# Kernel optimization log

Hardware: AMD Instinct MI355X
Metric: run time of the kernel (lower is better)

## Reference

```python
import jax, jax.numpy as jnp
import numpy as np

B_SZ, L, D_MODEL, D_STATE, D_CONV, EXPAND = 8, 2048, 512, 16, 4, 2
D_INNER = EXPAND * D_MODEL
DT_RANK = (D_MODEL + 15) // 16  # 32
ENC_IN, MARK_IN, C_OUT, PRED_LEN = 7, 4, 7, 96
IN_SIZE = ENC_IN + MARK_IN


def setup_inputs() -> dict:
    key = jax.random.key(0)
    ks = jax.random.split(key, 16)
    s = 0.02
    inp = {
        "x_enc": jax.random.normal(ks[0], (B_SZ, L, ENC_IN), jnp.float32),
        "x_mark_enc": jax.random.normal(ks[1], (B_SZ, L, MARK_IN), jnp.float32),
        "x_dec": jax.random.normal(ks[2], (B_SZ, PRED_LEN, ENC_IN), jnp.float32),
        "x_mark_dec": jax.random.normal(ks[3], (B_SZ, PRED_LEN, MARK_IN), jnp.float32),
        # input_transform
        "W_in": jax.random.normal(ks[4], (IN_SIZE, D_MODEL), jnp.float32) * s,
        "b_in": jnp.zeros((D_MODEL,), jnp.float32),
        # mamba in_proj (no bias)
        "W_inproj": jax.random.normal(ks[5], (D_MODEL, 2 * D_INNER), jnp.float32) * s,
        # depthwise causal conv
        "conv_w": jax.random.normal(ks[6], (D_INNER, D_CONV), jnp.float32) * s,
        "conv_b": jnp.zeros((D_INNER,), jnp.float32),
        # x_proj -> dt, B, C (no bias)
        "W_xproj": jax.random.normal(ks[7], (D_INNER, DT_RANK + 2 * D_STATE), jnp.float32) * s,
        # dt_proj
        "W_dt": jax.random.normal(ks[8], (DT_RANK, D_INNER), jnp.float32) * s,
        "b_dt": jnp.log(jnp.expm1(jnp.full((D_INNER,), 0.01, jnp.float32))),  # softplus-inv of ~0.01
        # S4D real init
        "A_log": jnp.log(jnp.broadcast_to(jnp.arange(1, D_STATE + 1, dtype=jnp.float32), (D_INNER, D_STATE))),
        "D": jnp.ones((D_INNER,), jnp.float32),
        # out_proj (no bias)
        "W_out": jax.random.normal(ks[9], (D_INNER, D_MODEL), jnp.float32) * s,
        # head
        "W_fc": jax.random.normal(ks[10], (D_MODEL, C_OUT), jnp.float32) * s,
        "b_fc": jnp.zeros((C_OUT,), jnp.float32),
    }
    return inp


def _mamba(x, W_inproj, conv_w, conv_b, W_xproj, W_dt, b_dt, A_log, D, W_out):
    # x: (B, L, d_model)
    xz = x @ W_inproj                      # (B, L, 2*d_inner)
    u, z = jnp.split(xz, 2, axis=-1)       # each (B, L, d_inner)
    # causal depthwise conv over time
    u_t = jnp.transpose(u, (0, 2, 1))      # (B, d_inner, L)
    conv = jax.lax.conv_general_dilated(
        u_t, conv_w[:, None, :], (1,), [(D_CONV - 1, 0)],
        dimension_numbers=("NCH", "OIH", "NCH"), feature_group_count=D_INNER)
    u = jax.nn.silu(jnp.transpose(conv, (0, 2, 1)) + conv_b)  # (B, L, d_inner)

    x_dbl = u @ W_xproj                    # (B, L, dt_rank + 2*d_state)
    dt_lo, Bmat, Cmat = jnp.split(x_dbl, [DT_RANK, DT_RANK + D_STATE], axis=-1)
    dt = jax.nn.softplus(dt_lo @ W_dt + b_dt)  # (B, L, d_inner)
    A = -jnp.exp(A_log)                    # (d_inner, d_state)

    def step(h, inp):
        dt_t, B_t, C_t, u_t = inp          # (B,d_inner),(B,d_state),(B,d_state),(B,d_inner)
        dA = jnp.exp(dt_t[:, :, None] * A)                       # (B, d_inner, d_state)
        dBu = dt_t[:, :, None] * B_t[:, None, :] * u_t[:, :, None]
        h = dA * h + dBu
        y = jnp.einsum("bds,bs->bd", h, C_t) + D * u_t
        return h, y

    h0 = jnp.zeros((x.shape[0], D_INNER, D_STATE), x.dtype)
    xs = (jnp.swapaxes(dt, 0, 1), jnp.swapaxes(Bmat, 0, 1),
          jnp.swapaxes(Cmat, 0, 1), jnp.swapaxes(u, 0, 1))
    _, ys = jax.lax.scan(step, h0, xs)     # ys: (L, B, d_inner)
    y = jnp.swapaxes(ys, 0, 1) * jax.nn.silu(z)
    return y @ W_out                       # (B, L, d_model)


def reference(x_enc, x_mark_enc, x_dec, x_mark_dec, W_in, b_in, W_inproj,
              conv_w, conv_b, W_xproj, W_dt, b_dt, A_log, D, W_out, W_fc, b_fc):
    x = jnp.concatenate([x_enc, x_mark_enc], axis=-1) @ W_in + b_in  # (B, L, d_model)
    x = _mamba(x, W_inproj, conv_w, conv_b, W_xproj, W_dt, b_dt, A_log, D, W_out)
    return x[:, -PRED_LEN:, :] @ W_fc + b_fc  # (B, pred_len, c_out)
```

## Files before the change

kernel.cpp:

```cpp
#include <hip/hip_runtime.h>
#include <math.h>

#define BB 8
#define LL 2048
#define DI 1024
#define NS 16
#define RK 32
#define NI 11
#define PRED 96
#define NC 7

static constexpr size_t OFF_WF   = 0;
static constexpr size_t OFF_BF   = 22528;
static constexpr size_t OFF_A2   = 24576;
static constexpr size_t OFF_WOF  = 40960;
static constexpr size_t OFF_CWT  = 48128;
static constexpr size_t OFF_WXH  = 52224;
static constexpr size_t OFF_WDTH = 84992;
static constexpr size_t OFF_DLH  = 101376;
static constexpr size_t OFF_BC   = 363520;
static constexpr size_t OFF_CC   = 625664;
static constexpr size_t OFF_YS   = 887808;
static constexpr size_t OFF_PB   = 1674240;
static constexpr size_t OFF_HB   = 5868544;
static constexpr size_t OFF_UH   = 10324992;

typedef __attribute__((ext_vector_type(8))) __bf16 bf16x8;
typedef __attribute__((ext_vector_type(8))) _Float16 f16x8;
typedef __attribute__((ext_vector_type(4))) float f32x4;

__device__ __forceinline__ float fexp2(float x) {
#if __has_builtin(__builtin_amdgcn_exp2f)
  return __builtin_amdgcn_exp2f(x);
#else
  return exp2f(x);
#endif
}
__device__ __forceinline__ unsigned short f2bf(float f) {
  unsigned int b = __float_as_uint(f);
  unsigned int r = (b + 0x7fffu + ((b >> 16) & 1u)) >> 16;
  return (unsigned short)r;
}
__device__ __forceinline__ unsigned short f2h_u(float f) {
  union { _Float16 h; unsigned short u; } c;
  c.h = (_Float16)f;
  return c.u;
}
__device__ __forceinline__ float h2f(unsigned short u) {
  union { unsigned short u; _Float16 h; } c;
  c.u = u;
  return (float)c.h;
}
__device__ __forceinline__ float softp(float a) {
  return (a > 15.f) ? a : __logf(1.f + __expf(a));
}

__global__ __launch_bounds__(256) void k_pre(
    const float* __restrict__ W_in, const float* __restrict__ b_in,
    const float* __restrict__ W_inproj, const float* __restrict__ conv_w,
    const float* __restrict__ W_xproj, const float* __restrict__ W_dt,
    const float* __restrict__ A_log,
    const float* __restrict__ W_out, const float* __restrict__ W_fc,
    float* __restrict__ ws) {
  int bid = blockIdx.x, tid = threadIdx.x;
  if (bid < 96) {
    int out = bid * 256 + tid;
    int r = out >> 11, c = out & 2047;
    const float* arow = (r < NI) ? (W_in + (size_t)r * 512) : b_in;
    float a0 = 0.f, a1 = 0.f, a2 = 0.f, a3 = 0.f;
    for (int k = 0; k < 512; k += 4) {
      a0 = fmaf(arow[k + 0], W_inproj[(size_t)(k + 0) * 2048 + c], a0);
      a1 = fmaf(arow[k + 1], W_inproj[(size_t)(k + 1) * 2048 + c], a1);
      a2 = fmaf(arow[k + 2], W_inproj[(size_t)(k + 2) * 2048 + c], a2);
      a3 = fmaf(arow[k + 3], W_inproj[(size_t)(k + 3) * 2048 + c], a3);
    }
    float acc = (a0 + a1) + (a2 + a3);
    if (r < NI) ws[OFF_WF + (size_t)r * 2048 + c] = acc;
    else ws[OFF_BF + c] = acc;
  } else if (bid < 160) {
    int idx = (bid - 96) * 256 + tid;
    ws[OFF_A2 + idx] = -expf(A_log[idx]) * 1.4426950408889634f;
  } else if (bid < 188) {
    int out = (bid - 160) * 256 + tid;
    int d = out / NC, cc = out - d * NC;
    float a0 = 0.f, a1 = 0.f, a2 = 0.f, a3 = 0.f;
    for (int k = 0; k < 512; k += 4) {
      a0 = fmaf(W_out[(size_t)d * 512 + k + 0], W_fc[(k + 0) * NC + cc], a0);
      a1 = fmaf(W_out[(size_t)d * 512 + k + 1], W_fc[(k + 1) * NC + cc], a1);
      a2 = fmaf(W_out[(size_t)d * 512 + k + 2], W_fc[(k + 2) * NC + cc], a2);
      a3 = fmaf(W_out[(size_t)d * 512 + k + 3], W_fc[(k + 3) * NC + cc], a3);
    }
    ws[OFF_WOF + out] = (a0 + a1) + (a2 + a3);
  } else if (bid < 204) {
    int idx = (bid - 188) * 256 + tid;
    int k = idx >> 10, dd = idx & 1023;
    ws[OFF_CWT + idx] = conv_w[dd * 4 + k];
  } else if (bid < 460) {
    int idx = (bid - 204) * 256 + tid;
    int c = idx >> 10, k = idx & 1023;
    unsigned short* wxh = (unsigned short*)(ws + OFF_WXH);
    wxh[idx] = f2bf(W_xproj[(size_t)k * 64 + c]);
  } else {
    int idx = (bid - 460) * 256 + tid;
    int dd = idx >> 5, k = idx & 31;
    unsigned short* wdh = (unsigned short*)(ws + OFF_WDTH);
    wdh[idx] = f2h_u(W_dt[(size_t)k * DI + dd]);
  }
}

__global__ __launch_bounds__(256) void k_u(
    const float* __restrict__ xe, const float* __restrict__ xm,
    const float* __restrict__ conv_b, float* __restrict__ ws) {
  __shared__ float scat[11][11];
  int bid = blockIdx.x, tid = threadIdx.x;
  int tg = bid >> 2, dq = bid & 3;
  int d = dq * 256 + tid;
  int b = tg >> 8;
  int t0 = (tg & 255) * 8;
  if (tid < 121) {
    int k = tid / 11, i = tid - k * 11;
    int tp = t0 - 3 + k;
    float v = 0.f;
    if (tp >= 0) v = (i < 7) ? xe[(size_t)(b * LL + tp) * 7 + i]
                             : xm[(size_t)(b * LL + tp) * 4 + (i - 7)];
    scat[k][i] = v;
  }
  __syncthreads();
  float wfv[NI];
#pragma unroll
  for (int i = 0; i < NI; ++i) wfv[i] = ws[OFF_WF + (size_t)i * 2048 + d];
  float bfu = ws[OFF_BF + d];
  float cwv[4];
#pragma unroll
  for (int k = 0; k < 4; ++k) cwv[k] = ws[OFF_CWT + k * 1024 + d];
  float cbv = conv_b[d];
  float xzv[11];
#pragma unroll
  for (int w2 = 0; w2 < 11; ++w2) {
    int tp = t0 - 3 + w2;
    float xz = bfu;
#pragma unroll
    for (int i = 0; i < NI; ++i) xz = fmaf(scat[w2][i], wfv[i], xz);
    xzv[w2] = (tp >= 0) ? xz : 0.f;
  }
  unsigned short* uhp = (unsigned short*)(ws + OFF_UH);
#pragma unroll
  for (int tt = 0; tt < 8; ++tt) {
    float acc = cbv;
#pragma unroll
    for (int k = 0; k < 4; ++k) acc = fmaf(cwv[k], xzv[tt + k], acc);
    float uval = acc / (1.f + __expf(-acc));
    uhp[(size_t)(b * LL + t0 + tt) * DI + d] = f2bf(uval);
  }
}

__global__ __launch_bounds__(256) void k_proj(float* __restrict__ ws) {
  __shared__ unsigned short su[64][72];
  __shared__ unsigned short sw[64][72];
  const unsigned short* uh  = (const unsigned short*)(ws + OFF_UH);
  const unsigned short* wxh = (const unsigned short*)(ws + OFF_WXH);
  int bid = blockIdx.x, tid = threadIdx.x;
  int r0 = bid * 64;
  int lane = tid & 63, w = tid >> 6;
  int srow = tid >> 3, skg = tid & 7;
  uint4 ru[2][2], rw[2][2];
  const ushort* ub0 = uh + (size_t)(r0 + srow) * DI + skg * 8;
  const ushort* wb0 = wxh + (size_t)srow * DI + skg * 8;
  ru[0][0] = *(const uint4*)(ub0);
  ru[0][1] = *(const uint4*)(ub0 + (size_t)32 * DI);
  rw[0][0] = *(const uint4*)(wb0);
  rw[0][1] = *(const uint4*)(wb0 + (size_t)32 * DI);
  ru[1][0] = *(const uint4*)(ub0 + 64);
  ru[1][1] = *(const uint4*)(ub0 + (size_t)32 * DI + 64);
  rw[1][0] = *(const uint4*)(wb0 + 64);
  rw[1][1] = *(const uint4*)(wb0 + (size_t)32 * DI + 64);
  f32x4 acc[4];
#pragma unroll
  for (int i = 0; i < 4; ++i) acc[i] = (f32x4){0.f, 0.f, 0.f, 0.f};
  int arow = w * 16 + (lane & 15);
  for (int kt = 0; kt < 16; ++kt) {
    int set = kt & 1;
    __syncthreads();
    *(uint4*)&su[srow][skg * 8]      = ru[set][0];
    *(uint4*)&su[srow + 32][skg * 8] = ru[set][1];
    *(uint4*)&sw[srow][skg * 8]      = rw[set][0];
    *(uint4*)&sw[srow + 32][skg * 8] = rw[set][1];
    __syncthreads();
    if (kt + 2 < 16) {
      int ko = (kt + 2) * 64;
      ru[set][0] = *(const uint4*)(ub0 + ko);
      ru[set][1] = *(const uint4*)(ub0 + (size_t)32 * DI + ko);
      rw[set][0] = *(const uint4*)(wb0 + ko);
      rw[set][1] = *(const uint4*)(wb0 + (size_t)32 * DI + ko);
    }
#pragma unroll
    for (int ks = 0; ks < 2; ++ks) {
      int koff = ks * 32 + (lane >> 4) * 8;
      bf16x8 av = *(const bf16x8*)&su[arow][koff];
#pragma unroll
      for (int nt = 0; nt < 4; ++nt) {
        bf16x8 bv = *(const bf16x8*)&sw[nt * 16 + (lane & 15)][koff];
        acc[nt] = __builtin_amdgcn_mfma_f32_16x16x32_bf16(av, bv, acc[nt], 0, 0, 0);
      }
    }
  }
  int orow = r0 + w * 16 + ((lane >> 4) << 2);
  int ocol = lane & 15;
  unsigned short* dlh = (unsigned short*)(ws + OFF_DLH);
#pragma unroll
  for (int reg = 0; reg < 4; ++reg) {
    size_t rr = orow + reg;
    dlh[rr * 32 + ocol]      = f2h_u(acc[0][reg]);
    dlh[rr * 32 + 16 + ocol] = f2h_u(acc[1][reg]);
    ws[OFF_BC + rr * NS + ocol] = acc[2][reg];
    ws[OFF_CC + rr * NS + ocol] = acc[3][reg];
  }
}

__global__ __launch_bounds__(128) void k_scan1(
    const float* __restrict__ b_dt, float* __restrict__ ws) {
  __shared__ unsigned short sdt[64][128];
  __shared__ unsigned short suu[64][128];
  __shared__ float sBB[64][16];
  int bid = blockIdx.x, tid = threadIdx.x;
  int b = bid >> 8, dgrp = (bid >> 5) & 7, ch = bid & 31;
  int d0 = dgrp * 128, t0 = ch * 64;
  size_t row0 = (size_t)b * LL + t0;
  const unsigned short* uh  = (const unsigned short*)(ws + OFF_UH) + row0 * DI + d0;
  const unsigned short* dlh = (const unsigned short*)(ws + OFF_DLH) + row0 * 32;
  const unsigned short* wdh = (const unsigned short*)(ws + OFF_WDTH);
  const float* Bp = ws + OFF_BC + row0 * NS;
  {
    int row = tid >> 1, q0 = (tid & 1) * 8;
    const uint4* src = (const uint4*)(uh + (size_t)row * DI) + q0;
    uint4* dst = (uint4*)&suu[row][0] + q0;
#pragma unroll
    for (int j = 0; j < 8; ++j) dst[j] = src[j];
  }
#pragma unroll
  for (int j = 0; j < 2; ++j) {
    int slot = tid * 2 + j, row = slot >> 2, q = slot & 3;
    *(float4*)&sBB[row][q * 4] = *(const float4*)&Bp[(size_t)row * NS + q * 4];
  }
  __syncthreads();
  {
    int lane = tid & 63, w = tid >> 6;
    int cl = lane & 15, kg = lane >> 4;
#pragma unroll
    for (int i = 0; i < 2; ++i) {
      int tq = 2 * w + i;
      f16x8 af = *(const f16x8*)&dlh[(size_t)(tq * 16 + cl) * 32 + kg * 8];
#pragma unroll
      for (int dq = 0; dq < 8; ++dq) {
        int dcol = d0 + dq * 16 + cl;
        f16x8 bf8 = *(const f16x8*)&wdh[(size_t)dcol * 32 + kg * 8];
        f32x4 acc = (f32x4){0.f, 0.f, 0.f, 0.f};
        acc = __builtin_amdgcn_mfma_f32_16x16x32_f16(af, bf8, acc, 0, 0, 0);
        float bdt = b_dt[dcol];
#pragma unroll
        for (int r = 0; r < 4; ++r)
          sdt[tq * 16 + kg * 4 + r][dq * 16 + cl] = f2h_u(softp(acc[r] + bdt));
      }
    }
  }
  __syncthreads();
  int d = d0 + tid;
  float a20 = ws[OFF_A2 + (size_t)d * NS];
  float h[16];
#pragma unroll
  for (int s = 0; s < 16; ++s) h[s] = 0.f;
  float S = 0.f;
  for (int t = 0; t < 64; ++t) {
    float dtv = h2f(sdt[t][tid]);
    float uv  = __uint_as_float((unsigned)suu[t][tid] << 16);
    float dtu = dtv * uv;
    S += dtv;
    float e1 = fexp2(dtv * a20);
    f32x4 b0 = *(const f32x4*)&sBB[t][0];
    f32x4 b1 = *(const f32x4*)&sBB[t][4];
    f32x4 b2 = *(const f32x4*)&sBB[t][8];
    f32x4 b3 = *(const f32x4*)&sBB[t][12];
    float dA = e1;
    h[0]  = fmaf(dA, h[0],  b0[0] * dtu); dA *= e1;
    h[1]  = fmaf(dA, h[1],  b0[1] * dtu); dA *= e1;
    h[2]  = fmaf(dA, h[2],  b0[2] * dtu); dA *= e1;
    h[3]  = fmaf(dA, h[3],  b0[3] * dtu); dA *= e1;
    h[4]  = fmaf(dA, h[4],  b1[0] * dtu); dA *= e1;
    h[5]  = fmaf(dA, h[5],  b1[1] * dtu); dA *= e1;
    h[6]  = fmaf(dA, h[6],  b1[2] * dtu); dA *= e1;
    h[7]  = fmaf(dA, h[7],  b1[3] * dtu); dA *= e1;
    h[8]  = fmaf(dA, h[8],  b2[0] * dtu); dA *= e1;
    h[9]  = fmaf(dA, h[9],  b2[1] * dtu); dA *= e1;
    h[10] = fmaf(dA, h[10], b2[2] * dtu); dA *= e1;
    h[11] = fmaf(dA, h[11], b2[3] * dtu); dA *= e1;
    h[12] = fmaf(dA, h[12], b3[0] * dtu); dA *= e1;
    h[13] = fmaf(dA, h[13], b3[1] * dtu); dA *= e1;
    h[14] = fmaf(dA, h[14], b3[2] * dtu); dA *= e1;
    h[15] = fmaf(dA, h[15], b3[3] * dtu);
  }
  float E1 = fexp2(S * a20);
  float P[16];
  float pp = E1;
#pragma unroll
  for (int s = 0; s < 16; ++s) { P[s] = pp; pp *= E1; }
  size_t base = (((size_t)b * 32 + ch) * 1024 + d) * 16;
#pragma unroll
  for (int q = 0; q < 4; ++q) {
    *(float4*)&ws[OFF_PB + base + q * 4] = *(float4*)&P[q * 4];
    *(float4*)&ws[OFF_HB + base + q * 4] = *(float4*)&h[q * 4];
  }
}

__global__ __launch_bounds__(128) void k_tail(
    const float* __restrict__ b_dt, const float* __restrict__ Dvec,
    float* __restrict__ ws) {
  __shared__ unsigned short sdt[64][128];
  __shared__ unsigned short suu[64][128];
  __shared__ float sBB[64][16];
  __shared__ float sCC[64][16];
  int bid = blockIdx.x, tid = threadIdx.x;
  int b = bid >> 4, dgrp = (bid >> 1) & 7, half = bid & 1;
  int d0 = dgrp * 128, t0 = (30 + half) * 64;
  size_t row0 = (size_t)b * LL + t0;
  const unsigned short* uh  = (const unsigned short*)(ws + OFF_UH) + row0 * DI + d0;
  const unsigned short* dlh = (const unsigned short*)(ws + OFF_DLH) + row0 * 32;
  const unsigned short* wdh = (const unsigned short*)(ws + OFF_WDTH);
  const float* Bp = ws + OFF_BC + row0 * NS;
  const float* Cp = ws + OFF_CC + row0 * NS;
  int d = d0 + tid;
  {
    int row = tid >> 1, q0 = (tid & 1) * 8;
    const uint4* src = (const uint4*)(uh + (size_t)row * DI) + q0;
    uint4* dst = (uint4*)&suu[row][0] + q0;
#pragma unroll
    for (int j = 0; j < 8; ++j) dst[j] = src[j];
  }
#pragma unroll
  for (int j = 0; j < 2; ++j) {
    int slot = tid * 2 + j, row = slot >> 2, q = slot & 3;
    *(float4*)&sBB[row][q * 4] = *(const float4*)&Bp[(size_t)row * NS + q * 4];
    *(float4*)&sCC[row][q * 4] = *(const float4*)&Cp[(size_t)row * NS + q * 4];
  }
  float h[16];
#pragma unroll
  for (int s = 0; s < 16; ++s) h[s] = 0.f;
  int nch = 30 + half;
  for (int c = 0; c < nch; ++c) {
    size_t cb = (((size_t)b * 32 + c) * 1024 + d) * 16;
#pragma unroll
    for (int q = 0; q < 4; ++q) {
      f32x4 Pv = *(const f32x4*)&ws[OFF_PB + cb + q * 4];
      f32x4 Hv = *(const f32x4*)&ws[OFF_HB + cb + q * 4];
#pragma unroll
      for (int j = 0; j < 4; ++j)
        h[q * 4 + j] = fmaf(Pv[j], h[q * 4 + j], Hv[j]);
    }
  }
  __syncthreads();
  {
    int lane = tid & 63, w = tid >> 6;
    int cl = lane & 15, kg = lane >> 4;
#pragma unroll
    for (int i = 0; i < 2; ++i) {
      int tq = 2 * w + i;
      f16x8 af = *(const f16x8*)&dlh[(size_t)(tq * 16 + cl) * 32 + kg * 8];
#pragma unroll
      for (int dq = 0; dq < 8; ++dq) {
        int dcol = d0 + dq * 16 + cl;
        f16x8 bf8 = *(const f16x8*)&wdh[(size_t)dcol * 32 + kg * 8];
        f32x4 acc = (f32x4){0.f, 0.f, 0.f, 0.f};
        acc = __builtin_amdgcn_mfma_f32_16x16x32_f16(af, bf8, acc, 0, 0, 0);
        float bdt = b_dt[dcol];
#pragma unroll
        for (int r = 0; r < 4; ++r)
          sdt[tq * 16 + kg * 4 + r][dq * 16 + cl] = f2h_u(softp(acc[r] + bdt));
      }
    }
  }
  __syncthreads();
  float a20 = ws[OFF_A2 + (size_t)d * NS];
  float Dv = Dvec[d];
  float* ysp = ws + OFF_YS;
  int tstart = half ? 0 : 32;
  for (int t = 0; t < 64; ++t) {
    float dtv = h2f(sdt[t][tid]);
    float uv  = __uint_as_float((unsigned)suu[t][tid] << 16);
    float dtu = dtv * uv;
    float e1 = fexp2(dtv * a20);
    f32x4 b0 = *(const f32x4*)&sBB[t][0];
    f32x4 b1 = *(const f32x4*)&sBB[t][4];
    f32x4 b2 = *(const f32x4*)&sBB[t][8];
    f32x4 b3 = *(const f32x4*)&sBB[t][12];
    float dA = e1;
    h[0]  = fmaf(dA, h[0],  b0[0] * dtu); dA *= e1;
    h[1]  = fmaf(dA, h[1],  b0[1] * dtu); dA *= e1;
    h[2]  = fmaf(dA, h[2],  b0[2] * dtu); dA *= e1;
    h[3]  = fmaf(dA, h[3],  b0[3] * dtu); dA *= e1;
    h[4]  = fmaf(dA, h[4],  b1[0] * dtu); dA *= e1;
    h[5]  = fmaf(dA, h[5],  b1[1] * dtu); dA *= e1;
    h[6]  = fmaf(dA, h[6],  b1[2] * dtu); dA *= e1;
    h[7]  = fmaf(dA, h[7],  b1[3] * dtu); dA *= e1;
    h[8]  = fmaf(dA, h[8],  b2[0] * dtu); dA *= e1;
    h[9]  = fmaf(dA, h[9],  b2[1] * dtu); dA *= e1;
    h[10] = fmaf(dA, h[10], b2[2] * dtu); dA *= e1;
    h[11] = fmaf(dA, h[11], b2[3] * dtu); dA *= e1;
    h[12] = fmaf(dA, h[12], b3[0] * dtu); dA *= e1;
    h[13] = fmaf(dA, h[13], b3[1] * dtu); dA *= e1;
    h[14] = fmaf(dA, h[14], b3[2] * dtu); dA *= e1;
    h[15] = fmaf(dA, h[15], b3[3] * dtu);
    if (t >= tstart) {
      f32x4 c0 = *(const f32x4*)&sCC[t][0];
      f32x4 c1 = *(const f32x4*)&sCC[t][4];
      f32x4 c2 = *(const f32x4*)&sCC[t][8];
      f32x4 c3 = *(const f32x4*)&sCC[t][12];
      float pv = h[0] * c0[0] + h[1] * c0[1] + h[2] * c0[2] + h[3] * c0[3]
               + h[4] * c1[0] + h[5] * c1[1] + h[6] * c1[2] + h[7] * c1[3]
               + h[8] * c2[0] + h[9] * c2[1] + h[10] * c2[2] + h[11] * c2[3]
               + h[12] * c3[0] + h[13] * c3[1] + h[14] * c3[2] + h[15] * c3[3];
      ysp[((size_t)(b * PRED + (t0 + t - (LL - PRED)))) * DI + d] = fmaf(Dv, uv, pv);
    }
  }
}

__global__ __launch_bounds__(256) void k_out(
    const float* __restrict__ xe, const float* __restrict__ xm,
    const float* __restrict__ b_fc, const float* __restrict__ ws,
    float* __restrict__ out) {
  __shared__ float scat[NI];
  __shared__ float sacc[4][NC];
  int bid = blockIdx.x, tid = threadIdx.x;
  int b = bid / PRED, p = bid - b * PRED;
  int t = LL - PRED + p;
  if (tid < NI) scat[tid] = (tid < 7) ? xe[(size_t)(b * LL + t) * 7 + tid]
                                      : xm[(size_t)(b * LL + t) * 4 + (tid - 7)];
  __syncthreads();
  const float* Wf  = ws + OFF_WF;
  const float* bf  = ws + OFF_BF;
  const float* Wof = ws + OFF_WOF;
  const float* ysp = ws + OFF_YS + ((size_t)bid) * DI;
  float acc[NC];
#pragma unroll
  for (int cc = 0; cc < NC; ++cc) acc[cc] = 0.f;
#pragma unroll
  for (int j = 0; j < 4; ++j) {
    int dd = tid + j * 256;
    float zv = bf[DI + dd];
#pragma unroll
    for (int i = 0; i < NI; ++i) zv = fmaf(scat[i], Wf[(size_t)i * 2048 + DI + dd], zv);
    float g = ysp[dd] * (zv / (1.f + __expf(-zv)));
#pragma unroll
    for (int cc = 0; cc < NC; ++cc) acc[cc] = fmaf(g, Wof[dd * NC + cc], acc[cc]);
  }
#pragma unroll
  for (int cc = 0; cc < NC; ++cc) {
    float v = acc[cc];
    for (int off = 32; off > 0; off >>= 1) v += __shfl_down(v, off);
    if ((tid & 63) == 0) sacc[tid >> 6][cc] = v;
  }
  __syncthreads();
  if (tid < NC)
    out[(size_t)bid * NC + tid] =
        sacc[0][tid] + sacc[1][tid] + sacc[2][tid] + sacc[3][tid] + b_fc[tid];
}

extern "C" void kernel_launch(void* const* d_in, const int* in_sizes, int n_in,
                              void* d_out, int out_size, void* d_ws, size_t ws_size,
                              hipStream_t stream) {
  const float* xe    = (const float*)d_in[0];
  const float* xm    = (const float*)d_in[1];
  const float* W_in  = (const float*)d_in[4];
  const float* b_in  = (const float*)d_in[5];
  const float* W_ip  = (const float*)d_in[6];
  const float* cw    = (const float*)d_in[7];
  const float* cb    = (const float*)d_in[8];
  const float* W_xp  = (const float*)d_in[9];
  const float* W_dt  = (const float*)d_in[10];
  const float* b_dt  = (const float*)d_in[11];
  const float* A_log = (const float*)d_in[12];
  const float* Dv    = (const float*)d_in[13];
  const float* W_out = (const float*)d_in[14];
  const float* W_fc  = (const float*)d_in[15];
  const float* b_fc  = (const float*)d_in[16];
  float* ws  = (float*)d_ws;
  float* out = (float*)d_out;

  k_pre  <<<588, 256, 0, stream>>>(W_in, b_in, W_ip, cw, W_xp, W_dt, A_log, W_out, W_fc, ws);
  k_u    <<<8192, 256, 0, stream>>>(xe, xm, cb, ws);
  k_proj <<<256, 256, 0, stream>>>(ws);
  k_scan1<<<2048, 128, 0, stream>>>(b_dt, ws);
  k_tail <<<128, 128, 0, stream>>>(b_dt, Dv, ws);
  k_out  <<<BB * PRED, 256, 0, stream>>>(xe, xm, b_fc, ws, out);
}
```

Baseline: 171.1 us.

## Move dt projection into k_proj and split scan states across threads

Computes the dt_proj MFMA plus softplus once in k_proj and writes a full fp16 dt tensor to global memory. k_scan1 and k_tail then load it instead of redoing the projection per block. k_scan1 now runs 256 threads, with each half handling 8 of the 16 states and using pow8 powers in place of the serial dA chain, which cuts the dependency chain length and doubles thread parallelism. The chunk P/H buffers are transposed to a state-major layout so reads are coalesced across d. The cost is an extra 32 MB fp16 dt write and read through global memory.

```diff
diff --git a/kernel.cpp b/kernel.cpp
--- a/kernel.cpp
+++ b/kernel.cpp
@@ -17,13 +17,13 @@
 static constexpr size_t OFF_CWT  = 48128;
 static constexpr size_t OFF_WXH  = 52224;
 static constexpr size_t OFF_WDTH = 84992;
-static constexpr size_t OFF_DLH  = 101376;
-static constexpr size_t OFF_BC   = 363520;
-static constexpr size_t OFF_CC   = 625664;
-static constexpr size_t OFF_YS   = 887808;
-static constexpr size_t OFF_PB   = 1674240;
-static constexpr size_t OFF_HB   = 5868544;
-static constexpr size_t OFF_UH   = 10324992;
+static constexpr size_t OFF_BC   = 101376;
+static constexpr size_t OFF_CC   = 363520;
+static constexpr size_t OFF_YS   = 625664;
+static constexpr size_t OFF_PB   = 1412096;
+static constexpr size_t OFF_HB   = 5606400;
+static constexpr size_t OFF_UH   = 9800704;
+static constexpr size_t OFF_DT   = 18189312;
 
 typedef __attribute__((ext_vector_type(8))) __bf16 bf16x8;
 typedef __attribute__((ext_vector_type(8))) _Float16 f16x8;
@@ -53,6 +53,24 @@
 }
 __device__ __forceinline__ float softp(float a) {
   return (a > 15.f) ? a : __logf(1.f + __expf(a));
+}
+__device__ __forceinline__ void pow8(float e1, int shalf, float* p) {
+  float c2 = e1 * e1, c4 = c2 * c2, c8 = c4 * c4;
+  float c3 = c2 * e1, c5 = c4 * e1, c6 = c4 * c2, c7 = c4 * c3;
+  if (shalf == 0) {
+    p[0] = e1; p[1] = c2; p[2] = c3; p[3] = c4;
+    p[4] = c5; p[5] = c6; p[6] = c7; p[7] = c8;
+  } else {
+    p[0] = c8 * e1; p[1] = c8 * c2; p[2] = c8 * c3; p[3] = c8 * c4;
+    p[4] = c8 * c5; p[5] = c8 * c6; p[6] = c8 * c7; p[7] = c8 * c8;
+  }
+}
+__device__ __forceinline__ void pow16(float e1, float* p) {
+  float c2 = e1 * e1, c4 = c2 * c2, c8 = c4 * c4;
+  p[0] = e1; p[1] = c2; p[2] = c2 * e1; p[3] = c4;
+  p[4] = c4 * e1; p[5] = c4 * c2; p[6] = c4 * p[2]; p[7] = c8;
+#pragma unroll
+  for (int j = 0; j < 8; ++j) p[8 + j] = c8 * p[j];
 }
 
 __global__ __launch_bounds__(256) void k_pre(
@@ -154,9 +172,11 @@
   }
 }
 
-__global__ __launch_bounds__(256) void k_proj(float* __restrict__ ws) {
+__global__ __launch_bounds__(256) void k_proj(
+    const float* __restrict__ b_dt, float* __restrict__ ws) {
   __shared__ unsigned short su[64][72];
   __shared__ unsigned short sw[64][72];
+  __shared__ _Float16 sdl2[64][40];
   const unsigned short* uh  = (const unsigned short*)(ws + OFF_UH);
   const unsigned short* wxh = (const unsigned short*)(ws + OFF_WXH);
   int bid = blockIdx.x, tid = threadIdx.x;
@@ -204,21 +224,41 @@
       }
     }
   }
-  int orow = r0 + w * 16 + ((lane >> 4) << 2);
+  int lrow = w * 16 + ((lane >> 4) << 2);
   int ocol = lane & 15;
-  unsigned short* dlh = (unsigned short*)(ws + OFF_DLH);
 #pragma unroll
   for (int reg = 0; reg < 4; ++reg) {
-    size_t rr = orow + reg;
-    dlh[rr * 32 + ocol]      = f2h_u(acc[0][reg]);
-    dlh[rr * 32 + 16 + ocol] = f2h_u(acc[1][reg]);
+    size_t rr = (size_t)(r0 + lrow + reg);
+    sdl2[lrow + reg][ocol]      = (_Float16)acc[0][reg];
+    sdl2[lrow + reg][ocol + 16] = (_Float16)acc[1][reg];
     ws[OFF_BC + rr * NS + ocol] = acc[2][reg];
     ws[OFF_CC + rr * NS + ocol] = acc[3][reg];
   }
-}
-
-__global__ __launch_bounds__(128) void k_scan1(
-    const float* __restrict__ b_dt, float* __restrict__ ws) {
+  __syncthreads();
+  int cl = lane & 15, kg = lane >> 4;
+  f16x8 af[4];
+#pragma unroll
+  for (int tt = 0; tt < 4; ++tt)
+    af[tt] = *(const f16x8*)&sdl2[tt * 16 + cl][kg * 8];
+  unsigned short* dtg = (unsigned short*)(ws + OFF_DT);
+  const unsigned short* wdh = (const unsigned short*)(ws + OFF_WDTH);
+  for (int dj = 0; dj < 16; ++dj) {
+    int dcol = (dj * 4 + w) * 16 + cl;
+    f16x8 bf8 = *(const f16x8*)&wdh[(size_t)dcol * 32 + kg * 8];
+    float bdt = b_dt[dcol];
+#pragma unroll
+    for (int tt = 0; tt < 4; ++tt) {
+      f32x4 a2 = (f32x4){0.f, 0.f, 0.f, 0.f};
+      a2 = __builtin_amdgcn_mfma_f32_16x16x32_f16(af[tt], bf8, a2, 0, 0, 0);
+#pragma unroll
+      for (int r = 0; r < 4; ++r)
+        dtg[(size_t)(r0 + tt * 16 + kg * 4 + r) * DI + dcol] =
+            f2h_u(softp(a2[r] + bdt));
+    }
+  }
+}
+
+__global__ __launch_bounds__(256) void k_scan1(float* __restrict__ ws) {
   __shared__ unsigned short sdt[64][128];
   __shared__ unsigned short suu[64][128];
   __shared__ float sBB[64][16];
@@ -227,93 +267,58 @@
   int d0 = dgrp * 128, t0 = ch * 64;
   size_t row0 = (size_t)b * LL + t0;
   const unsigned short* uh  = (const unsigned short*)(ws + OFF_UH) + row0 * DI + d0;
-  const unsigned short* dlh = (const unsigned short*)(ws + OFF_DLH) + row0 * 32;
-  const unsigned short* wdh = (const unsigned short*)(ws + OFF_WDTH);
+  const unsigned short* dtg = (const unsigned short*)(ws + OFF_DT) + row0 * DI + d0;
   const float* Bp = ws + OFF_BC + row0 * NS;
+#pragma unroll
+  for (int j = 0; j < 4; ++j) {
+    int i = j * 256 + tid, row = i >> 4, q = i & 15;
+    *(uint4*)&suu[row][q * 8] = *(const uint4*)(uh + (size_t)row * DI + q * 8);
+    *(uint4*)&sdt[row][q * 8] = *(const uint4*)(dtg + (size_t)row * DI + q * 8);
+  }
   {
-    int row = tid >> 1, q0 = (tid & 1) * 8;
-    const uint4* src = (const uint4*)(uh + (size_t)row * DI) + q0;
-    uint4* dst = (uint4*)&suu[row][0] + q0;
-#pragma unroll
-    for (int j = 0; j < 8; ++j) dst[j] = src[j];
-  }
-#pragma unroll
-  for (int j = 0; j < 2; ++j) {
-    int slot = tid * 2 + j, row = slot >> 2, q = slot & 3;
+    int row = tid >> 2, q = tid & 3;
     *(float4*)&sBB[row][q * 4] = *(const float4*)&Bp[(size_t)row * NS + q * 4];
   }
   __syncthreads();
-  {
-    int lane = tid & 63, w = tid >> 6;
-    int cl = lane & 15, kg = lane >> 4;
-#pragma unroll
-    for (int i = 0; i < 2; ++i) {
-      int tq = 2 * w + i;
-      f16x8 af = *(const f16x8*)&dlh[(size_t)(tq * 16 + cl) * 32 + kg * 8];
-#pragma unroll
-      for (int dq = 0; dq < 8; ++dq) {
-        int dcol = d0 + dq * 16 + cl;
-        f16x8 bf8 = *(const f16x8*)&wdh[(size_t)dcol * 32 + kg * 8];
-        f32x4 acc = (f32x4){0.f, 0.f, 0.f, 0.f};
-        acc = __builtin_amdgcn_mfma_f32_16x16x32_f16(af, bf8, acc, 0, 0, 0);
-        float bdt = b_dt[dcol];
-#pragma unroll
-        for (int r = 0; r < 4; ++r)
-          sdt[tq * 16 + kg * 4 + r][dq * 16 + cl] = f2h_u(softp(acc[r] + bdt));
-      }
-    }
-  }
-  __syncthreads();
-  int d = d0 + tid;
+  int dl = tid & 127, shalf = tid >> 7, s0 = shalf * 8;
+  int d = d0 + dl;
   float a20 = ws[OFF_A2 + (size_t)d * NS];
-  float h[16];
-#pragma unroll
-  for (int s = 0; s < 16; ++s) h[s] = 0.f;
+  float h[8];
+#pragma unroll
+  for (int j = 0; j < 8; ++j) h[j] = 0.f;
   float S = 0.f;
   for (int t = 0; t < 64; ++t) {
-    float dtv = h2f(sdt[t][tid]);
-    float uv  = __uint_as_float((unsigned)suu[t][tid] << 16);
+    float dtv = h2f(sdt[t][dl]);
+    float uv  = __uint_as_float((unsigned)suu[t][dl] << 16);
     float dtu = dtv * uv;
     S += dtv;
     float e1 = fexp2(dtv * a20);
-    f32x4 b0 = *(const f32x4*)&sBB[t][0];
-    f32x4 b1 = *(const f32x4*)&sBB[t][4];
-    f32x4 b2 = *(const f32x4*)&sBB[t][8];
-    f32x4 b3 = *(const f32x4*)&sBB[t][12];
-    float dA = e1;
-    h[0]  = fmaf(dA, h[0],  b0[0] * dtu); dA *= e1;
-    h[1]  = fmaf(dA, h[1],  b0[1] * dtu); dA *= e1;
-    h[2]  = fmaf(dA, h[2],  b0[2] * dtu); dA *= e1;
-    h[3]  = fmaf(dA, h[3],  b0[3] * dtu); dA *= e1;
-    h[4]  = fmaf(dA, h[4],  b1[0] * dtu); dA *= e1;
-    h[5]  = fmaf(dA, h[5],  b1[1] * dtu); dA *= e1;
-    h[6]  = fmaf(dA, h[6],  b1[2] * dtu); dA *= e1;
-    h[7]  = fmaf(dA, h[7],  b1[3] * dtu); dA *= e1;
-    h[8]  = fmaf(dA, h[8],  b2[0] * dtu); dA *= e1;
-    h[9]  = fmaf(dA, h[9],  b2[1] * dtu); dA *= e1;
-    h[10] = fmaf(dA, h[10], b2[2] * dtu); dA *= e1;
-    h[11] = fmaf(dA, h[11], b2[3] * dtu); dA *= e1;
-    h[12] = fmaf(dA, h[12], b3[0] * dtu); dA *= e1;
-    h[13] = fmaf(dA, h[13], b3[1] * dtu); dA *= e1;
-    h[14] = fmaf(dA, h[14], b3[2] * dtu); dA *= e1;
-    h[15] = fmaf(dA, h[15], b3[3] * dtu);
+    float p[8];
+    pow8(e1, shalf, p);
+    f32x4 b0 = *(const f32x4*)&sBB[t][s0];
+    f32x4 b1 = *(const f32x4*)&sBB[t][s0 + 4];
+    h[0] = fmaf(p[0], h[0], b0[0] * dtu);
+    h[1] = fmaf(p[1], h[1], b0[1] * dtu);
+    h[2] = fmaf(p[2], h[2], b0[2] * dtu);
+    h[3] = fmaf(p[3], h[3], b0[3] * dtu);
+    h[4] = fmaf(p[4], h[4], b1[0] * dtu);
+    h[5] = fmaf(p[5], h[5], b1[1] * dtu);
+    h[6] = fmaf(p[6], h[6], b1[2] * dtu);
+    h[7] = fmaf(p[7], h[7], b1[3] * dtu);
   }
   float E1 = fexp2(S * a20);
-  float P[16];
-  float pp = E1;
-#pragma unroll
-  for (int s = 0; s < 16; ++s) { P[s] = pp; pp *= E1; }
-  size_t base = (((size_t)b * 32 + ch) * 1024 + d) * 16;
-#pragma unroll
-  for (int q = 0; q < 4; ++q) {
-    *(float4*)&ws[OFF_PB + base + q * 4] = *(float4*)&P[q * 4];
-    *(float4*)&ws[OFF_HB + base + q * 4] = *(float4*)&h[q * 4];
+  float P[8];
+  pow8(E1, shalf, P);
+  size_t base = (((size_t)b * 32 + ch) * NS + s0) * 1024 + d;
+#pragma unroll
+  for (int j = 0; j < 8; ++j) {
+    ws[OFF_PB + base + (size_t)j * 1024] = P[j];
+    ws[OFF_HB + base + (size_t)j * 1024] = h[j];
   }
 }
 
 __global__ __launch_bounds__(128) void k_tail(
-    const float* __restrict__ b_dt, const float* __restrict__ Dvec,
-    float* __restrict__ ws) {
+    const float* __restrict__ Dvec, float* __restrict__ ws) {
   __shared__ unsigned short sdt[64][128];
   __shared__ unsigned short suu[64][128];
   __shared__ float sBB[64][16];
@@ -323,59 +328,32 @@
   int d0 = dgrp * 128, t0 = (30 + half) * 64;
   size_t row0 = (size_t)b * LL + t0;
   const unsigned short* uh  = (const unsigned short*)(ws + OFF_UH) + row0 * DI + d0;
-  const unsigned short* dlh = (const unsigned short*)(ws + OFF_DLH) + row0 * 32;
-  const unsigned short* wdh = (const unsigned short*)(ws + OFF_WDTH);
+  const unsigned short* dtg = (const unsigned short*)(ws + OFF_DT) + row0 * DI + d0;
   const float* Bp = ws + OFF_BC + row0 * NS;
   const float* Cp = ws + OFF_CC + row0 * NS;
-  int d = d0 + tid;
-  {
-    int row = tid >> 1, q0 = (tid & 1) * 8;
-    const uint4* src = (const uint4*)(uh + (size_t)row * DI) + q0;
-    uint4* dst = (uint4*)&suu[row][0] + q0;
-#pragma unroll
-    for (int j = 0; j < 8; ++j) dst[j] = src[j];
+#pragma unroll
+  for (int j = 0; j < 8; ++j) {
+    int i = j * 128 + tid, row = i >> 4, q = i & 15;
+    *(uint4*)&suu[row][q * 8] = *(const uint4*)(uh + (size_t)row * DI + q * 8);
+    *(uint4*)&sdt[row][q * 8] = *(const uint4*)(dtg + (size_t)row * DI + q * 8);
   }
 #pragma unroll
   for (int j = 0; j < 2; ++j) {
-    int slot = tid * 2 + j, row = slot >> 2, q = slot & 3;
+    int i = j * 128 + tid, row = i >> 2, q = i & 3;
     *(float4*)&sBB[row][q * 4] = *(const float4*)&Bp[(size_t)row * NS + q * 4];
     *(float4*)&sCC[row][q * 4] = *(const float4*)&Cp[(size_t)row * NS + q * 4];
   }
+  int d = d0 + tid;
   float h[16];
 #pragma unroll
   for (int s = 0; s < 16; ++s) h[s] = 0.f;
   int nch = 30 + half;
   for (int c = 0; c < nch; ++c) {
-    size_t cb = (((size_t)b * 32 + c) * 1024 + d) * 16;
-#pragma unroll
-    for (int q = 0; q < 4; ++q) {
-      f32x4 Pv = *(const f32x4*)&ws[OFF_PB + cb + q * 4];
-      f32x4 Hv = *(const f32x4*)&ws[OFF_HB + cb + q * 4];
-#pragma unroll
-      for (int j = 0; j < 4; ++j)
-        h[q * 4 + j] = fmaf(Pv[j], h[q * 4 + j], Hv[j]);
-    }
-  }
-  __syncthreads();
-  {
-    int lane = tid & 63, w = tid >> 6;
-    int cl = lane & 15, kg = lane >> 4;
-#pragma unroll
-    for (int i = 0; i < 2; ++i) {
-      int tq = 2 * w + i;
-      f16x8 af = *(const f16x8*)&dlh[(size_t)(tq * 16 + cl) * 32 + kg * 8];
-#pragma unroll
-      for (int dq = 0; dq < 8; ++dq) {
-        int dcol = d0 + dq * 16 + cl;
-        f16x8 bf8 = *(const f16x8*)&wdh[(size_t)dcol * 32 + kg * 8];
-        f32x4 acc = (f32x4){0.f, 0.f, 0.f, 0.f};
-        acc = __builtin_amdgcn_mfma_f32_16x16x32_f16(af, bf8, acc, 0, 0, 0);
-        float bdt = b_dt[dcol];
-#pragma unroll
-        for (int r = 0; r < 4; ++r)
-          sdt[tq * 16 + kg * 4 + r][dq * 16 + cl] = f2h_u(softp(acc[r] + bdt));
-      }
-    }
+    size_t cb = ((size_t)b * 32 + c) * NS * 1024 + d;
+#pragma unroll
+    for (int s = 0; s < 16; ++s)
+      h[s] = fmaf(ws[OFF_PB + cb + (size_t)s * 1024], h[s],
+                  ws[OFF_HB + cb + (size_t)s * 1024]);
   }
   __syncthreads();
   float a20 = ws[OFF_A2 + (size_t)d * NS];
@@ -387,27 +365,19 @@
     float uv  = __uint_as_float((unsigned)suu[t][tid] << 16);
     float dtu = dtv * uv;
     float e1 = fexp2(dtv * a20);
+    float p[16];
+    pow16(e1, p);
     f32x4 b0 = *(const f32x4*)&sBB[t][0];
     f32x4 b1 = *(const f32x4*)&sBB[t][4];
     f32x4 b2 = *(const f32x4*)&sBB[t][8];
     f32x4 b3 = *(const f32x4*)&sBB[t][12];
-    float dA = e1;
-    h[0]  = fmaf(dA, h[0],  b0[0] * dtu); dA *= e1;
-    h[1]  = fmaf(dA, h[1],  b0[1] * dtu); dA *= e1;
-    h[2]  = fmaf(dA, h[2],  b0[2] * dtu); dA *= e1;
-    h[3]  = fmaf(dA, h[3],  b0[3] * dtu); dA *= e1;
-    h[4]  = fmaf(dA, h[4],  b1[0] * dtu); dA *= e1;
-    h[5]  = fmaf(dA, h[5],  b1[1] * dtu); dA *= e1;
-    h[6]  = fmaf(dA, h[6],  b1[2] * dtu); dA *= e1;
-    h[7]  = fmaf(dA, h[7],  b1[3] * dtu); dA *= e1;
-    h[8]  = fmaf(dA, h[8],  b2[0] * dtu); dA *= e1;
-    h[9]  = fmaf(dA, h[9],  b2[1] * dtu); dA *= e1;
-    h[10] = fmaf(dA, h[10], b2[2] * dtu); dA *= e1;
-    h[11] = fmaf(dA, h[11], b2[3] * dtu); dA *= e1;
-    h[12] = fmaf(dA, h[12], b3[0] * dtu); dA *= e1;
-    h[13] = fmaf(dA, h[13], b3[1] * dtu); dA *= e1;
-    h[14] = fmaf(dA, h[14], b3[2] * dtu); dA *= e1;
-    h[15] = fmaf(dA, h[15], b3[3] * dtu);
+#pragma unroll
+    for (int j = 0; j < 4; ++j) {
+      h[j]      = fmaf(p[j],      h[j],      b0[j] * dtu);
+      h[j + 4]  = fmaf(p[j + 4],  h[j + 4],  b1[j] * dtu);
+      h[j + 8]  = fmaf(p[j + 8],  h[j + 8],  b2[j] * dtu);
+      h[j + 12] = fmaf(p[j + 12], h[j + 12], b3[j] * dtu);
+    }
     if (t >= tstart) {
       f32x4 c0 = *(const f32x4*)&sCC[t][0];
       f32x4 c1 = *(const f32x4*)&sCC[t][4];
@@ -486,8 +456,8 @@
 
   k_pre  <<<588, 256, 0, stream>>>(W_in, b_in, W_ip, cw, W_xp, W_dt, A_log, W_out, W_fc, ws);
   k_u    <<<8192, 256, 0, stream>>>(xe, xm, cb, ws);
-  k_proj <<<256, 256, 0, stream>>>(ws);
-  k_scan1<<<2048, 128, 0, stream>>>(b_dt, ws);
-  k_tail <<<128, 128, 0, stream>>>(b_dt, Dv, ws);
+  k_proj <<<256, 256, 0, stream>>>(b_dt, ws);
+  k_scan1<<<2048, 256, 0, stream>>>(ws);
+  k_tail <<<128, 128, 0, stream>>>(Dv, ws);
   k_out  <<<BB * PRED, 256, 0, stream>>>(xe, xm, b_fc, ws, out);
 }
```

After: 178.1 us. 1.04x slower.
